# Performance work log

Measured on AMD Instinct MI355X. Metric: run time of the kernel, lower is better.

## Reference

```python
import jax, jax.numpy as jnp
import numpy as np

CHANNELS = 256
C8 = CHANNELS // 8


def setup_inputs() -> dict:
    key = jax.random.key(0)
    ks = jax.random.split(key, 7)
    b, c, h, w = 4, CHANNELS, 64, 64
    x = jax.random.normal(ks[0], (b, c, h, w), dtype=jnp.float32)
    # 1x1 conv weights stored as [out_ch, in_ch] (kernel is 1x1)
    s = 1.0 / np.sqrt(c)
    wq = jax.random.uniform(ks[1], (C8, c), jnp.float32, -s, s)
    bq = jax.random.uniform(ks[2], (C8,), jnp.float32, -s, s)
    wk = jax.random.uniform(ks[3], (C8, c), jnp.float32, -s, s)
    bk = jax.random.uniform(ks[4], (C8,), jnp.float32, -s, s)
    wv = jax.random.uniform(ks[5], (c, c), jnp.float32, -s, s)
    bv = jax.random.uniform(ks[6], (c,), jnp.float32, -s, s)
    return {"x": x, "wq": wq, "bq": bq, "wk": wk, "bk": bk, "wv": wv, "bv": bv}


def reference(x, wq, bq, wk, bk, wv, bv):
    b, c, h, w = x.shape
    n = h * w
    xf = x.reshape(b, c, n)                                  # (b, c, n)
    q = jnp.einsum('oc,bcn->bon', wq, xf) + bq[None, :, None]  # (b, c/8, n)
    k = jnp.einsum('oc,bcn->bon', wk, xf) + bk[None, :, None]  # (b, c/8, n)
    v = jnp.einsum('oc,bcn->bon', wv, xf) + bv[None, :, None]  # (b, c, n)
    # attention[b, i, j] = softmax_j( q[:, :, i] . k[:, :, j] )
    scores = jnp.einsum('bdi,bdj->bij', q, k)                # (b, n, n)
    attn = jax.nn.softmax(scores, axis=-1)
    # out = value @ attention^T  -> out[b, c, i] = sum_j v[b, c, j] * attn[b, i, j]
    out = jnp.einsum('bcj,bij->bci', v, attn)                # (b, c, n)
    return out.reshape(b, c, h, w) + x
```

## Files before the change

### kernel.cpp

```cpp
#include <hip/hip_runtime.h>
#include <hip/hip_bf16.h>
#include <stdint.h>

#define CH 256
#define D8 32
#define NN 4096

typedef __attribute__((ext_vector_type(8))) short short8;
typedef __attribute__((ext_vector_type(4))) float f32x4;

#define MFMA16(a,b,c) __builtin_amdgcn_mfma_f32_16x16x32_bf16(a,b,c,0,0,0)

static __device__ __forceinline__ short f2bf(float f) {
  union { float f; uint32_t u; } v; v.f = f;
  uint32_t r = v.u + 0x7fffu + ((v.u >> 16) & 1u);
  return (short)(r >> 16);
}
static __device__ __forceinline__ float bf2f(short h) {
  union { float f; uint32_t u; } v; v.u = ((uint32_t)(uint16_t)h) << 16;
  return v.f;
}

__global__ __launch_bounds__(256) void prep_kernel(
    const float* __restrict__ x,
    const float* __restrict__ wq, const float* __restrict__ bq,
    const float* __restrict__ wk, const float* __restrict__ bk,
    const float* __restrict__ wv, const float* __restrict__ bv,
    short* __restrict__ xT, short* __restrict__ WQb,
    short* __restrict__ WKb, short* __restrict__ WVb,
    float* __restrict__ BQ, float* __restrict__ BK, float* __restrict__ BV)
{
  int blk = blockIdx.x, t = threadIdx.x;
  if (blk >= 1024) {
    int idx = (blk - 1024) * 256 + t;
    const float LOG2E = 1.4426950408889634f;
    for (int i = idx; i < D8 * CH; i += 2048) WQb[i] = f2bf(wq[i] * LOG2E);
    for (int i = idx; i < D8 * CH; i += 2048) WKb[i] = f2bf(wk[i]);
    for (int i = idx; i < CH * CH; i += 2048) WVb[i] = f2bf(wv[i]);
    if (idx < D8) { BQ[idx] = bq[idx] * LOG2E; BK[idx] = bk[idx]; }
    if (idx < CH) BV[idx] = bv[idx];
    return;
  }
  int b = blk >> 8, ct = (blk >> 6) & 3, nt = blk & 63;
  __shared__ short T[64][65];
  int j = t & 63, i0 = t >> 6;
  const float* xb = x + ((size_t)b * CH + ct * 64) * NN + nt * 64;
  #pragma unroll
  for (int k = 0; k < 16; ++k) {
    int i = k * 4 + i0;
    T[i][j] = f2bf(xb[(size_t)i * NN + j]);
  }
  __syncthreads();
  short* xTb = xT + ((size_t)b * NN + nt * 64) * CH + ct * 64;
  #pragma unroll
  for (int k = 0; k < 16; ++k) {
    int n = k * 4 + i0;
    xTb[(size_t)n * CH + j] = T[j][n];
  }
}

__global__ __launch_bounds__(256) void proj_kernel(
    const short* __restrict__ xT,
    const short* __restrict__ WQb, const short* __restrict__ WKb,
    const short* __restrict__ WVb,
    const float* __restrict__ BQ, const float* __restrict__ BK,
    const float* __restrict__ BV,
    short* __restrict__ Qh, short* __restrict__ Ql,
    short* __restrict__ Kh, short* __restrict__ Kl,
    short* __restrict__ Vo)
{
  int blk = blockIdx.x, t = threadIdx.x;
  int b = blk >> 6, pt = blk & 63;
  int w = t >> 6, lane = t & 63, g = lane >> 4, lr = lane & 15;
  int p0 = pt * 64 + w * 16;
  __shared__ short Vl[CH][66];

  const short* xrow = xT + ((size_t)b * NN + p0 + lr) * CH + g * 8;
  short8 a[8];
  #pragma unroll
  for (int s = 0; s < 8; ++s) a[s] = *(const short8*)(xrow + s * 32);

  const f32x4 zf = {0.f, 0.f, 0.f, 0.f};

  #pragma unroll
  for (int qk = 0; qk < 2; ++qk) {
    const short* W = qk ? WKb : WQb;
    const float* Bs = qk ? BK : BQ;
    short* Outh = qk ? Kh : Qh;
    short* Outl = qk ? Kl : Ql;
    #pragma unroll
    for (int tq = 0; tq < 2; ++tq) {
      f32x4 acc = zf;
      #pragma unroll
      for (int s = 0; s < 8; ++s) {
        short8 bb = *(const short8*)(W + (size_t)(tq * 16 + lr) * CH + s * 32 + g * 8);
        acc = MFMA16(a[s], bb, acc);
      }
      int o = tq * 16 + lr;
      float bias = Bs[o];
      #pragma unroll
      for (int r = 0; r < 4; ++r) {
        int pos = p0 + g * 4 + r;
        float val = acc[r] + bias;
        short hi = f2bf(val);
        Outh[((size_t)b * NN + pos) * D8 + o] = hi;
        Outl[((size_t)b * NN + pos) * D8 + o] = f2bf(val - bf2f(hi));
      }
    }
  }

#define VSTEP(TV, CUR, NXT) do { \
    int _tn = ((TV) + 1) & 15; \
    _Pragma("unroll") \
    for (int s = 0; s < 8; ++s) \
      NXT[s] = *(const short8*)(WVb + (size_t)(_tn * 16 + lr) * CH + s * 32 + g * 8); \
    f32x4 acc = zf; \
    _Pragma("unroll") \
    for (int s = 0; s < 8; ++s) acc = MFMA16(a[s], CUR[s], acc); \
    int o = (TV) * 16 + lr; \
    float bias = BV[o]; \
    _Pragma("unroll") \
    for (int r = 0; r < 4; ++r) Vl[o][w * 16 + g * 4 + r] = f2bf(acc[r] + bias); \
  } while (0)

  short8 bA[8], bB[8];
  #pragma unroll
  for (int s = 0; s < 8; ++s)
    bA[s] = *(const short8*)(WVb + (size_t)lr * CH + s * 32 + g * 8);
  #pragma unroll
  for (int tv2 = 0; tv2 < 8; ++tv2) {
    VSTEP(2 * tv2, bA, bB);
    VSTEP(2 * tv2 + 1, bB, bA);
  }
#undef VSTEP

  __syncthreads();
  int pj = t & 63, orow = t >> 6;
  short* Vb = Vo + (size_t)b * CH * NN + pt * 64 + pj;
  #pragma unroll
  for (int oi = 0; oi < 64; ++oi) {
    int o = orow * 64 + oi;
    Vb[(size_t)o * NN] = Vl[o][pj];
  }
}

__global__ __launch_bounds__(256) void attn_kernel(
    const short* __restrict__ Qh, const short* __restrict__ Ql,
    const short* __restrict__ Kh, const short* __restrict__ Kl,
    const short* __restrict__ V, const float* __restrict__ x,
    float* __restrict__ out)
{
  int blk = blockIdx.x, t = threadIdx.x;
  int xcd = blk & 7, idx = blk >> 3;
  int b = xcd >> 1;
  int qt = ((xcd & 1) << 5) + idx;
  int q0 = qt * 64;
  int w = t >> 6, lane = t & 63, g = lane >> 4, lr = lane & 15;
  int cw0 = w * 64;

  union Smem {
    struct {
      short P[2][64 * 64];
      float scale[2][64];
      int   flags[2][4];
    } lp;
    float O[CH][67];
  };
  __shared__ Smem sm;
  __shared__ float l_lds[64];

  const short* Qhb = Qh + (size_t)b * NN * D8;
  const short* Qlb = Ql + (size_t)b * NN * D8;
  const short* Khb = Kh + (size_t)b * NN * D8;
  const short* Klb = Kl + (size_t)b * NN * D8;
  const short* Vb = V + (size_t)b * CH * NN;

  short8 aqh = *(const short8*)(Qhb + (size_t)(q0 + w * 16 + lr) * D8 + g * 8);
  short8 aql = *(const short8*)(Qlb + (size_t)(q0 + w * 16 + lr) * D8 + g * 8);

  const f32x4 zf = {0.f, 0.f, 0.f, 0.f};
  f32x4 O[4][4];
  #pragma unroll
  for (int i = 0; i < 4; ++i)
    #pragma unroll
    for (int j = 0; j < 4; ++j) O[i][j] = zf;
  float m[4] = {-INFINITY, -INFINITY, -INFINITY, -INFINITY};
  float l[4] = {0.f, 0.f, 0.f, 0.f};

  char* Pbase0 = (char*)&sm.lp.P[0][0];
  char* Pbase1 = (char*)&sm.lp.P[1][0];

#define LOADK(KH, KL, KIDX) do { \
    int _k0 = (KIDX) * 64; \
    _Pragma("unroll") \
    for (int _nt = 0; _nt < 4; ++_nt) { \
      size_t _off = (size_t)(_k0 + _nt * 16 + lr) * D8 + g * 8; \
      KH[_nt] = *(const short8*)(Khb + _off); \
      KL[_nt] = *(const short8*)(Klb + _off); \
    } \
  } while (0)

#define LOADV(VV, KIDX) do { \
    int _k0 = (KIDX) * 64; \
    _Pragma("unroll") \
    for (int _ss = 0; _ss < 2; ++_ss) \
      _Pragma("unroll") \
      for (int _ci = 0; _ci < 4; ++_ci) \
        VV[_ss * 4 + _ci] = *(const short8*)(Vb + \
            (size_t)(cw0 + _ci * 16 + lr) * NN + _k0 + _ss * 32 + g * 8); \
  } while (0)

#define STEP(KB, KH, KL, VV, NKH, NKL, NVV) do { \
    int _buf = (KB) & 1; \
    char* _Pb = _buf ? Pbase1 : Pbase0; \
     \
    f32x4 S[4]; \
    _Pragma("unroll") \
    for (int nt = 0; nt < 4; ++nt) { \
      f32x4 s_ = MFMA16(aql, KH[nt], zf); \
      s_ = MFMA16(aqh, KL[nt], s_); \
      s_ = MFMA16(aqh, KH[nt], s_); \
      S[nt] = s_; \
    } \
     \
    int _kn = ((KB) + 1) & 63; \
    LOADK(NKH, NKL, _kn); \
    LOADV(NVV, _kn); \
     \
    float sc[4]; \
    bool upd = false; \
    _Pragma("unroll") \
    for (int r = 0; r < 4; ++r) { \
      float v = fmaxf(fmaxf(S[0][r], S[1][r]), fmaxf(S[2][r], S[3][r])); \
      v = fmaxf(v, __shfl_xor(v, 1)); \
      v = fmaxf(v, __shfl_xor(v, 2)); \
      v = fmaxf(v, __shfl_xor(v, 4)); \
      v = fmaxf(v, __shfl_xor(v, 8)); \
      bool u = v > m[r] + 8.0f;                   \
      upd |= u; \
      float mn = u ? v : m[r]; \
      sc[r] = __builtin_amdgcn_exp2f(m[r] - mn); \
      m[r] = mn; \
    } \
    bool anyupd = __any((int)upd); \
    float rsum[4] = {0.f, 0.f, 0.f, 0.f}; \
    short pb[4][4]; \
    _Pragma("unroll") \
    for (int nt = 0; nt < 4; ++nt) \
      _Pragma("unroll") \
      for (int r = 0; r < 4; ++r) { \
        float p = __builtin_amdgcn_exp2f(S[nt][r] - m[r]); \
        rsum[r] += p; \
        pb[nt][r] = f2bf(p); \
      } \
    _Pragma("unroll") \
    for (int r = 0; r < 4; ++r) { \
      float v = rsum[r]; \
      v += __shfl_xor(v, 1); v += __shfl_xor(v, 2); \
      v += __shfl_xor(v, 4); v += __shfl_xor(v, 8); \
      l[r] = l[r] * sc[r] + v; \
    } \
     \
    _Pragma("unroll") \
    for (int nt = 0; nt < 4; ++nt) \
      _Pragma("unroll") \
      for (int r = 0; r < 4; ++r) { \
        int qloc = w * 16 + g * 4 + r; \
        int kk = nt * 16 + lr; \
        int off = (qloc * 128 + kk * 2) ^ ((qloc & 7) << 4); \
        *(short*)(_Pb + off) = pb[nt][r]; \
      } \
    if (lr == 0) { \
      _Pragma("unroll") \
      for (int r = 0; r < 4; ++r) \
        sm.lp.scale[_buf][w * 16 + g * 4 + r] = sc[r]; \
    } \
    if (lane == 0) sm.lp.flags[_buf][w] = anyupd ? 1 : 0; \
    __syncthreads();                              \
    int need = sm.lp.flags[_buf][0] | sm.lp.flags[_buf][1] | \
               sm.lp.flags[_buf][2] | sm.lp.flags[_buf][3]; \
    if (need) { \
      _Pragma("unroll") \
      for (int mi = 0; mi < 4; ++mi) \
        _Pragma("unroll") \
        for (int r = 0; r < 4; ++r) { \
          float s = sm.lp.scale[_buf][mi * 16 + g * 4 + r]; \
          _Pragma("unroll") \
          for (int ci = 0; ci < 4; ++ci) O[mi][ci][r] *= s; \
        } \
    } \
     \
    _Pragma("unroll") \
    for (int ss = 0; ss < 2; ++ss) { \
      short8 ap[4]; \
      _Pragma("unroll") \
      for (int mi = 0; mi < 4; ++mi) { \
        int row = mi * 16 + lr; \
        int off = (row * 128 + (ss * 32 + g * 8) * 2) ^ ((row & 7) << 4); \
        ap[mi] = *(const short8*)(_Pb + off); \
      } \
      _Pragma("unroll") \
      for (int ci = 0; ci < 4; ++ci) { \
        _Pragma("unroll") \
        for (int mi = 0; mi < 4; ++mi) \
          O[mi][ci] = MFMA16(ap[mi], VV[ss * 4 + ci], O[mi][ci]); \
      } \
    } \
  } while (0)

  short8 khA[4], klA[4], vA[8], khB[4], klB[4], vB[8];
  LOADK(khA, klA, 0);
  LOADV(vA, 0);
  #pragma unroll 1
  for (int kb2 = 0; kb2 < 32; ++kb2) {
    STEP(2 * kb2,     khA, klA, vA, khB, klB, vB);
    STEP(2 * kb2 + 1, khB, klB, vB, khA, klA, vA);
  }
#undef STEP
#undef LOADK
#undef LOADV

  if (lr == 0) {
    #pragma unroll
    for (int r = 0; r < 4; ++r)
      l_lds[w * 16 + g * 4 + r] = l[r];
  }
  __syncthreads();
  #pragma unroll
  for (int mi = 0; mi < 4; ++mi)
    #pragma unroll
    for (int ci = 0; ci < 4; ++ci) {
      int ch = cw0 + ci * 16 + lr;
      #pragma unroll
      for (int r = 0; r < 4; ++r)
        sm.O[ch][mi * 16 + g * 4 + r] = O[mi][ci][r];
    }
  __syncthreads();
  int q = t & 63, orow = t >> 6;
  float linv = 1.0f / l_lds[q];
  const float* xb = x + (size_t)b * CH * NN + q0 + q;
  float* ob = out + (size_t)b * CH * NN + q0 + q;
  #pragma unroll
  for (int oi = 0; oi < 64; ++oi) {
    int ch = orow * 64 + oi;
    ob[(size_t)ch * NN] = sm.O[ch][q] * linv + xb[(size_t)ch * NN];
  }
}

extern "C" void kernel_launch(void* const* d_in, const int* in_sizes, int n_in,
                              void* d_out, int out_size, void* d_ws, size_t ws_size,
                              hipStream_t stream) {
  const float* x  = (const float*)d_in[0];
  const float* wq = (const float*)d_in[1];
  const float* bq = (const float*)d_in[2];
  const float* wk = (const float*)d_in[3];
  const float* bk = (const float*)d_in[4];
  const float* wv = (const float*)d_in[5];
  const float* bv = (const float*)d_in[6];
  char* ws = (char*)d_ws;
  short* xT  = (short*)(ws);
  short* Qh  = (short*)(ws + 8388608);
  short* Ql  = (short*)(ws + 9437184);
  short* Kh  = (short*)(ws + 10485760);
  short* Kl  = (short*)(ws + 11534336);
  short* Vo  = (short*)(ws + 12582912);
  short* WQb = (short*)(ws + 20971520);
  short* WKb = (short*)(ws + 20987904);
  short* WVb = (short*)(ws + 21004288);
  float* BQ  = (float*)(ws + 21135360);
  float* BK  = (float*)(ws + 21135488);
  float* BV  = (float*)(ws + 21135616);

  prep_kernel<<<1032, 256, 0, stream>>>(x, wq, bq, wk, bk, wv, bv,
                                        xT, WQb, WKb, WVb, BQ, BK, BV);
  proj_kernel<<<256, 256, 0, stream>>>(xT, WQb, WKb, WVb, BQ, BK, BV,
                                       Qh, Ql, Kh, Kl, Vo);
  attn_kernel<<<256, 256, 0, stream>>>(Qh, Ql, Kh, Kl, Vo, x, (float*)d_out);
}
```

Measured before the change: 238.1 us.

## Split attention into score and PV warp roles, widen proj grid

The attention kernel now launches 512 threads per block. Four warps compute scores and softmax and write P to shared memory, and all eight warps each do the PV MFMA for 32 channels instead of 64. This halves the per-warp PV accumulator register footprint and adds more waves to hide latency, and it raises MFMA priority during the PV phase. The projection kernel is regridded to 1024 blocks of 16 positions, with each warp handling five output tiles, which removes the big LDS transpose in favour of small per-warp transposes. The risks are that the score warps become the critical path while the PV-only warps sit idle at the barrier, and that the per-warp V stores are small and narrow.

```diff
diff --git a/kernel.cpp b/kernel.cpp
--- a/kernel.cpp
+++ b/kernel.cpp
@@ -7,6 +7,7 @@
 #define NN 4096
 
 typedef __attribute__((ext_vector_type(8))) short short8;
+typedef __attribute__((ext_vector_type(4))) short s16x4;
 typedef __attribute__((ext_vector_type(4))) float f32x4;
 
 #define MFMA16(a,b,c) __builtin_amdgcn_mfma_f32_16x16x32_bf16(a,b,c,0,0,0)
@@ -70,10 +71,10 @@
     short* __restrict__ Vo)
 {
   int blk = blockIdx.x, t = threadIdx.x;
-  int b = blk >> 6, pt = blk & 63;
+  int b = blk >> 8, pt = blk & 255;
   int w = t >> 6, lane = t & 63, g = lane >> 4, lr = lane & 15;
-  int p0 = pt * 64 + w * 16;
-  __shared__ short Vl[CH][66];
+  int p0 = pt * 16;
+  __shared__ short Vt[4][16][20];
 
   const short* xrow = xT + ((size_t)b * NN + p0 + lr) * CH + g * 8;
   short8 a[8];
@@ -83,68 +84,43 @@
   const f32x4 zf = {0.f, 0.f, 0.f, 0.f};
 
   #pragma unroll
-  for (int qk = 0; qk < 2; ++qk) {
-    const short* W = qk ? WKb : WQb;
-    const float* Bs = qk ? BK : BQ;
-    short* Outh = qk ? Kh : Qh;
-    short* Outl = qk ? Kl : Ql;
+  for (int i = 0; i < 5; ++i) {
+    int tt = w * 5 + i;
+    const short* W; const float* Bs; int tloc;
+    if (tt < 2)      { W = WQb; Bs = BQ; tloc = tt; }
+    else if (tt < 4) { W = WKb; Bs = BK; tloc = tt - 2; }
+    else             { W = WVb; Bs = BV; tloc = tt - 4; }
+    f32x4 acc = zf;
     #pragma unroll
-    for (int tq = 0; tq < 2; ++tq) {
-      f32x4 acc = zf;
-      #pragma unroll
-      for (int s = 0; s < 8; ++s) {
-        short8 bb = *(const short8*)(W + (size_t)(tq * 16 + lr) * CH + s * 32 + g * 8);
-        acc = MFMA16(a[s], bb, acc);
-      }
-      int o = tq * 16 + lr;
-      float bias = Bs[o];
+    for (int s = 0; s < 8; ++s) {
+      short8 bb = *(const short8*)(W + (size_t)(tloc * 16 + lr) * CH + s * 32 + g * 8);
+      acc = MFMA16(a[s], bb, acc);
+    }
+    int o = tloc * 16 + lr;
+    float bias = Bs[o];
+    if (tt < 4) {
+      short* Oh = (tt < 2) ? Qh : Kh;
+      short* Ol = (tt < 2) ? Ql : Kl;
       #pragma unroll
       for (int r = 0; r < 4; ++r) {
         int pos = p0 + g * 4 + r;
         float val = acc[r] + bias;
         short hi = f2bf(val);
-        Outh[((size_t)b * NN + pos) * D8 + o] = hi;
-        Outl[((size_t)b * NN + pos) * D8 + o] = f2bf(val - bf2f(hi));
+        Oh[((size_t)b * NN + pos) * D8 + o] = hi;
+        Ol[((size_t)b * NN + pos) * D8 + o] = f2bf(val - bf2f(hi));
       }
+    } else {
+      #pragma unroll
+      for (int r = 0; r < 4; ++r)
+        Vt[w][lr][g * 4 + r] = f2bf(acc[r] + bias);
+      int row = lane >> 2, c4 = (lane & 3) * 4;
+      s16x4 vv = *(const s16x4*)&Vt[w][row][c4];
+      *(s16x4*)(Vo + ((size_t)b * CH + tloc * 16 + row) * NN + p0 + c4) = vv;
     }
   }
-
-#define VSTEP(TV, CUR, NXT) do { \
-    int _tn = ((TV) + 1) & 15; \
-    _Pragma("unroll") \
-    for (int s = 0; s < 8; ++s) \
-      NXT[s] = *(const short8*)(WVb + (size_t)(_tn * 16 + lr) * CH + s * 32 + g * 8); \
-    f32x4 acc = zf; \
-    _Pragma("unroll") \
-    for (int s = 0; s < 8; ++s) acc = MFMA16(a[s], CUR[s], acc); \
-    int o = (TV) * 16 + lr; \
-    float bias = BV[o]; \
-    _Pragma("unroll") \
-    for (int r = 0; r < 4; ++r) Vl[o][w * 16 + g * 4 + r] = f2bf(acc[r] + bias); \
-  } while (0)
-
-  short8 bA[8], bB[8];
-  #pragma unroll
-  for (int s = 0; s < 8; ++s)
-    bA[s] = *(const short8*)(WVb + (size_t)lr * CH + s * 32 + g * 8);
-  #pragma unroll
-  for (int tv2 = 0; tv2 < 8; ++tv2) {
-    VSTEP(2 * tv2, bA, bB);
-    VSTEP(2 * tv2 + 1, bB, bA);
-  }
-#undef VSTEP
-
-  __syncthreads();
-  int pj = t & 63, orow = t >> 6;
-  short* Vb = Vo + (size_t)b * CH * NN + pt * 64 + pj;
-  #pragma unroll
-  for (int oi = 0; oi < 64; ++oi) {
-    int o = orow * 64 + oi;
-    Vb[(size_t)o * NN] = Vl[o][pj];
-  }
-}
-
-__global__ __launch_bounds__(256) void attn_kernel(
+}
+
+__global__ __launch_bounds__(512) void attn_kernel(
     const short* __restrict__ Qh, const short* __restrict__ Ql,
     const short* __restrict__ Kh, const short* __restrict__ Kl,
     const short* __restrict__ V, const float* __restrict__ x,
@@ -156,7 +132,9 @@
   int qt = ((xcd & 1) << 5) + idx;
   int q0 = qt * 64;
   int w = t >> 6, lane = t & 63, g = lane >> 4, lr = lane & 15;
-  int cw0 = w * 64;
+  int wS = w & 3;
+  bool isS = (w < 4);
+  int cw0 = w * 32;
 
   union Smem {
     struct {
@@ -175,15 +153,18 @@
   const short* Klb = Kl + (size_t)b * NN * D8;
   const short* Vb = V + (size_t)b * CH * NN;
 
-  short8 aqh = *(const short8*)(Qhb + (size_t)(q0 + w * 16 + lr) * D8 + g * 8);
-  short8 aql = *(const short8*)(Qlb + (size_t)(q0 + w * 16 + lr) * D8 + g * 8);
+  short8 aqh, aql;
+  if (isS) {
+    aqh = *(const short8*)(Qhb + (size_t)(q0 + wS * 16 + lr) * D8 + g * 8);
+    aql = *(const short8*)(Qlb + (size_t)(q0 + wS * 16 + lr) * D8 + g * 8);
+  }
 
   const f32x4 zf = {0.f, 0.f, 0.f, 0.f};
-  f32x4 O[4][4];
+  f32x4 O[4][2];
   #pragma unroll
   for (int i = 0; i < 4; ++i)
     #pragma unroll
-    for (int j = 0; j < 4; ++j) O[i][j] = zf;
+    for (int j = 0; j < 2; ++j) O[i][j] = zf;
   float m[4] = {-INFINITY, -INFINITY, -INFINITY, -INFINITY};
   float l[4] = {0.f, 0.f, 0.f, 0.f};
 
@@ -205,77 +186,80 @@
     _Pragma("unroll") \
     for (int _ss = 0; _ss < 2; ++_ss) \
       _Pragma("unroll") \
-      for (int _ci = 0; _ci < 4; ++_ci) \
-        VV[_ss * 4 + _ci] = *(const short8*)(Vb + \
+      for (int _ci = 0; _ci < 2; ++_ci) \
+        VV[_ss * 2 + _ci] = *(const short8*)(Vb + \
             (size_t)(cw0 + _ci * 16 + lr) * NN + _k0 + _ss * 32 + g * 8); \
   } while (0)
 
 #define STEP(KB, KH, KL, VV, NKH, NKL, NVV) do { \
     int _buf = (KB) & 1; \
     char* _Pb = _buf ? Pbase1 : Pbase0; \
-     \
-    f32x4 S[4]; \
-    _Pragma("unroll") \
-    for (int nt = 0; nt < 4; ++nt) { \
-      f32x4 s_ = MFMA16(aql, KH[nt], zf); \
-      s_ = MFMA16(aqh, KL[nt], s_); \
-      s_ = MFMA16(aqh, KH[nt], s_); \
-      S[nt] = s_; \
+    int _kn = ((KB) + 1) & 63; \
+    if (isS) { \
+       \
+      f32x4 S[4]; \
+      _Pragma("unroll") \
+      for (int nt = 0; nt < 4; ++nt) { \
+        f32x4 s_ = MFMA16(aql, KH[nt], zf); \
+        s_ = MFMA16(aqh, KL[nt], s_); \
+        s_ = MFMA16(aqh, KH[nt], s_); \
+        S[nt] = s_; \
+      } \
+      LOADK(NKH, NKL, _kn); \
+      LOADV(NVV, _kn); \
+       \
+      float sc[4]; \
+      bool upd = false; \
+      _Pragma("unroll") \
+      for (int r = 0; r < 4; ++r) { \
+        float v = fmaxf(fmaxf(S[0][r], S[1][r]), fmaxf(S[2][r], S[3][r])); \
+        v = fmaxf(v, __shfl_xor(v, 1)); \
+        v = fmaxf(v, __shfl_xor(v, 2)); \
+        v = fmaxf(v, __shfl_xor(v, 4)); \
+        v = fmaxf(v, __shfl_xor(v, 8)); \
+        bool u = v > m[r] + 8.0f;                 \
+        upd |= u; \
+        float mn = u ? v : m[r]; \
+        sc[r] = __builtin_amdgcn_exp2f(m[r] - mn); \
+        m[r] = mn; \
+      } \
+      bool anyupd = __any((int)upd); \
+      float rsum[4] = {0.f, 0.f, 0.f, 0.f}; \
+      short pb[4][4]; \
+      _Pragma("unroll") \
+      for (int nt = 0; nt < 4; ++nt) \
+        _Pragma("unroll") \
+        for (int r = 0; r < 4; ++r) { \
+          float p = __builtin_amdgcn_exp2f(S[nt][r] - m[r]); \
+          rsum[r] += p; \
+          pb[nt][r] = f2bf(p); \
+        } \
+      _Pragma("unroll") \
+      for (int r = 0; r < 4; ++r) { \
+        float v = rsum[r]; \
+        v += __shfl_xor(v, 1); v += __shfl_xor(v, 2); \
+        v += __shfl_xor(v, 4); v += __shfl_xor(v, 8); \
+        l[r] = l[r] * sc[r] + v; \
+      } \
+       \
+      _Pragma("unroll") \
+      for (int nt = 0; nt < 4; ++nt) \
+        _Pragma("unroll") \
+        for (int r = 0; r < 4; ++r) { \
+          int qloc = wS * 16 + g * 4 + r; \
+          int kk = nt * 16 + lr; \
+          int off = (qloc * 128 + kk * 2) ^ ((qloc & 7) << 4); \
+          *(short*)(_Pb + off) = pb[nt][r]; \
+        } \
+      if (lr == 0) { \
+        _Pragma("unroll") \
+        for (int r = 0; r < 4; ++r) \
+          sm.lp.scale[_buf][wS * 16 + g * 4 + r] = sc[r]; \
+      } \
+      if (lane == 0) sm.lp.flags[_buf][wS] = anyupd ? 1 : 0; \
+    } else { \
+      LOADV(NVV, _kn); \
     } \
-     \
-    int _kn = ((KB) + 1) & 63; \
-    LOADK(NKH, NKL, _kn); \
-    LOADV(NVV, _kn); \
-     \
-    float sc[4]; \
-    bool upd = false; \
-    _Pragma("unroll") \
-    for (int r = 0; r < 4; ++r) { \
-      float v = fmaxf(fmaxf(S[0][r], S[1][r]), fmaxf(S[2][r], S[3][r])); \
-      v = fmaxf(v, __shfl_xor(v, 1)); \
-      v = fmaxf(v, __shfl_xor(v, 2)); \
-      v = fmaxf(v, __shfl_xor(v, 4)); \
-      v = fmaxf(v, __shfl_xor(v, 8)); \
-      bool u = v > m[r] + 8.0f;                   \
-      upd |= u; \
-      float mn = u ? v : m[r]; \
-      sc[r] = __builtin_amdgcn_exp2f(m[r] - mn); \
-      m[r] = mn; \
-    } \
-    bool anyupd = __any((int)upd); \
-    float rsum[4] = {0.f, 0.f, 0.f, 0.f}; \
-    short pb[4][4]; \
-    _Pragma("unroll") \
-    for (int nt = 0; nt < 4; ++nt) \
-      _Pragma("unroll") \
-      for (int r = 0; r < 4; ++r) { \
-        float p = __builtin_amdgcn_exp2f(S[nt][r] - m[r]); \
-        rsum[r] += p; \
-        pb[nt][r] = f2bf(p); \
-      } \
-    _Pragma("unroll") \
-    for (int r = 0; r < 4; ++r) { \
-      float v = rsum[r]; \
-      v += __shfl_xor(v, 1); v += __shfl_xor(v, 2); \
-      v += __shfl_xor(v, 4); v += __shfl_xor(v, 8); \
-      l[r] = l[r] * sc[r] + v; \
-    } \
-     \
-    _Pragma("unroll") \
-    for (int nt = 0; nt < 4; ++nt) \
-      _Pragma("unroll") \
-      for (int r = 0; r < 4; ++r) { \
-        int qloc = w * 16 + g * 4 + r; \
-        int kk = nt * 16 + lr; \
-        int off = (qloc * 128 + kk * 2) ^ ((qloc & 7) << 4); \
-        *(short*)(_Pb + off) = pb[nt][r]; \
-      } \
-    if (lr == 0) { \
-      _Pragma("unroll") \
-      for (int r = 0; r < 4; ++r) \
-        sm.lp.scale[_buf][w * 16 + g * 4 + r] = sc[r]; \
-    } \
-    if (lane == 0) sm.lp.flags[_buf][w] = anyupd ? 1 : 0; \
     __syncthreads();                              \
     int need = sm.lp.flags[_buf][0] | sm.lp.flags[_buf][1] | \
                sm.lp.flags[_buf][2] | sm.lp.flags[_buf][3]; \
@@ -286,10 +270,11 @@
         for (int r = 0; r < 4; ++r) { \
           float s = sm.lp.scale[_buf][mi * 16 + g * 4 + r]; \
           _Pragma("unroll") \
-          for (int ci = 0; ci < 4; ++ci) O[mi][ci][r] *= s; \
+          for (int ci = 0; ci < 2; ++ci) O[mi][ci][r] *= s; \
         } \
     } \
      \
+    __builtin_amdgcn_s_setprio(1); \
     _Pragma("unroll") \
     for (int ss = 0; ss < 2; ++ss) { \
       short8 ap[4]; \
@@ -300,16 +285,17 @@
         ap[mi] = *(const short8*)(_Pb + off); \
       } \
       _Pragma("unroll") \
-      for (int ci = 0; ci < 4; ++ci) { \
+      for (int ci = 0; ci < 2; ++ci) { \
         _Pragma("unroll") \
         for (int mi = 0; mi < 4; ++mi) \
-          O[mi][ci] = MFMA16(ap[mi], VV[ss * 4 + ci], O[mi][ci]); \
+          O[mi][ci] = MFMA16(ap[mi], VV[ss * 2 + ci], O[mi][ci]); \
       } \
     } \
+    __builtin_amdgcn_s_setprio(0); \
   } while (0)
 
-  short8 khA[4], klA[4], vA[8], khB[4], klB[4], vB[8];
-  LOADK(khA, klA, 0);
+  short8 khA[4], klA[4], vA[4], khB[4], klB[4], vB[4];
+  if (isS) LOADK(khA, klA, 0);
   LOADV(vA, 0);
   #pragma unroll 1
   for (int kb2 = 0; kb2 < 32; ++kb2) {
@@ -320,29 +306,29 @@
 #undef LOADK
 #undef LOADV
 
-  if (lr == 0) {
+  if (isS && lr == 0) {
     #pragma unroll
     for (int r = 0; r < 4; ++r)
-      l_lds[w * 16 + g * 4 + r] = l[r];
+      l_lds[wS * 16 + g * 4 + r] = l[r];
   }
   __syncthreads();
   #pragma unroll
   for (int mi = 0; mi < 4; ++mi)
     #pragma unroll
-    for (int ci = 0; ci < 4; ++ci) {
+    for (int ci = 0; ci < 2; ++ci) {
       int ch = cw0 + ci * 16 + lr;
       #pragma unroll
       for (int r = 0; r < 4; ++r)
         sm.O[ch][mi * 16 + g * 4 + r] = O[mi][ci][r];
     }
   __syncthreads();
-  int q = t & 63, orow = t >> 6;
+  int q = t & 63, crow = t >> 6;
   float linv = 1.0f / l_lds[q];
   const float* xb = x + (size_t)b * CH * NN + q0 + q;
   float* ob = out + (size_t)b * CH * NN + q0 + q;
   #pragma unroll
-  for (int oi = 0; oi < 64; ++oi) {
-    int ch = orow * 64 + oi;
+  for (int oi = 0; oi < 32; ++oi) {
+    int ch = crow * 32 + oi;
     ob[(size_t)ch * NN] = sm.O[ch][q] * linv + xb[(size_t)ch * NN];
   }
 }
@@ -373,7 +359,7 @@
 
   prep_kernel<<<1032, 256, 0, stream>>>(x, wq, bq, wk, bk, wv, bv,
                                         xT, WQb, WKb, WVb, BQ, BK, BV);
-  proj_kernel<<<256, 256, 0, stream>>>(xT, WQb, WKb, WVb, BQ, BK, BV,
-                                       Qh, Ql, Kh, Kl, Vo);
-  attn_kernel<<<256, 256, 0, stream>>>(Qh, Ql, Kh, Kl, Vo, x, (float*)d_out);
-}
+  proj_kernel<<<1024, 256, 0, stream>>>(xT, WQb, WKb, WVb, BQ, BK, BV,
+                                        Qh, Ql, Kh, Kl, Vo);
+  attn_kernel<<<256, 512, 0, stream>>>(Qh, Ql, Kh, Kl, Vo, x, (float*)d_out);
+}
```

Measured after the change: 218.3 us. 8.3% less time.
